# Optimization experiments

Measured on AMD Instinct MI355X. Metric: run time of the kernel, lower is better.

The kernel has to match this reference:

```python
import math
import jax, jax.numpy as jnp
import numpy as np

HIDDEN = 1024
HEADS = 16
HEAD_DIM = HIDDEN // HEADS
PRIME = 7
MAX_ITERS = 10
ENT_THRESH = 0.2
PRIME_SCALE = 1.0 / math.sqrt(PRIME * HEAD_DIM)
EPS = 1e-6


def setup_inputs() -> dict:
    key = jax.random.key(0)
    ks = jax.random.split(key, 6)
    B, S = 2, 2048
    w = 0.02
    return {
        "hidden_states": jax.random.normal(ks[0], (B, S, HIDDEN), jnp.float32),
        "q_w": jax.random.normal(ks[1], (HIDDEN, HIDDEN), jnp.float32) * w,
        "q_b": jnp.zeros((HIDDEN,), jnp.float32),
        "k_w": jax.random.normal(ks[2], (HIDDEN, HIDDEN), jnp.float32) * w,
        "k_b": jnp.zeros((HIDDEN,), jnp.float32),
        "v_w": jax.random.normal(ks[3], (HIDDEN, HIDDEN), jnp.float32) * w,
        "v_b": jnp.zeros((HIDDEN,), jnp.float32),
        "o_w": jax.random.normal(ks[4], (HIDDEN, HIDDEN), jnp.float32) * w,
        "o_b": jnp.zeros((HIDDEN,), jnp.float32),
        "attention_mask": jnp.ones((B, S), jnp.int32),
    }


def _split_heads(x):
    B, S, _ = x.shape
    return x.reshape(B, S, HEADS, HEAD_DIM).transpose(0, 2, 1, 3)


def reference(hidden_states, q_w, q_b, k_w, k_b, v_w, v_b, o_w, o_b, attention_mask):
    B, S, _ = hidden_states.shape
    # projections (torch Linear: x @ W^T + b)
    q = _split_heads(hidden_states @ q_w.T + q_b) * PRIME_SCALE  # [B,H,S,hd]
    k = _split_heads(hidden_states @ k_w.T + k_b)
    v = _split_heads(hidden_states @ v_w.T + v_b)

    scores = jnp.einsum("bhqd,bhkd->bhqk", q, k)  # [B,H,S,S]
    mask = attention_mask[:, None, None, :]
    scores = jnp.where(mask == 0, -jnp.inf, scores)
    attn = jax.nn.softmax(scores, axis=-1)  # dropout p=0 (eval)

    base = jnp.einsum("bhqk,bhkd->bhqd", attn, v)  # attention_weights @ v

    # entropy of the (fixed) attention weights: [B,H]
    entropy = -jnp.sum(attn * jnp.log(attn + EPS), axis=-1).mean(axis=-1)
    avg_entropy = entropy.mean()

    # loop never changes attn, so entropy is constant: either break at i=1 or run all
    full = base
    for i in range(1, MAX_ITERS):
        blend = 1.0 / (1.0 + math.exp(-i / MAX_ITERS))          # sigmoid(i/max)
        res_scale = 0.5 + 0.5 * blend                            # resonance scale
        full = (1.0 - blend) * full + blend * (res_scale * base)

    out_heads = jnp.where(avg_entropy < ENT_THRESH, base, full)  # [B,H,S,hd]

    merged = out_heads.transpose(0, 2, 1, 3).reshape(B, S, HIDDEN)
    return merged @ o_w.T + o_b
```

## Files before the change

kernel.cpp:

```cpp
#include <hip/hip_runtime.h>
#include <hip/hip_bf16.h>
#include <stdint.h>


#define PRIME_SCALE 0.047245559126654356f
#define LOG2E       1.4426950408889634f
#define LN2         0.6931471805599453f
#define QSCALE      (PRIME_SCALE * LOG2E)
#define BLEND_C     0.85096556f

#if __has_builtin(__builtin_amdgcn_exp2f)
#define EXP2(x) __builtin_amdgcn_exp2f(x)
#else
#define EXP2(x) exp2f(x)
#endif

typedef __attribute__((ext_vector_type(8))) short short8;
typedef __attribute__((ext_vector_type(4))) float f32x4;

__device__ __forceinline__ unsigned short f2bf(float x) {
    union { float f; unsigned int u; } v; v.f = x;
    unsigned int r = (v.u + 0x7fffu + ((v.u >> 16) & 1u)) >> 16;
    return (unsigned short)r;
}
__device__ __forceinline__ unsigned short f2bf_fast(float x) {
    union { float f; unsigned int u; } v; v.f = x;
    return (unsigned short)((v.u + 0x8000u) >> 16);
}
__device__ __forceinline__ float bf2f(unsigned short x) {
    union { unsigned int u; float f; } v; v.u = ((unsigned int)x) << 16;
    return v.f;
}
__device__ __forceinline__ unsigned cvtpk_bf16(float lo, float hi) {
    unsigned r;
    asm("v_cvt_pk_bf16_f32 %0, %1, %2" : "=v"(r) : "v"(lo), "v"(hi));
    return r;
}

__device__ __forceinline__ void glds16(const unsigned short* g, unsigned short* l) {
    __builtin_amdgcn_global_load_lds((const __attribute__((address_space(1))) unsigned int*)g,
                                     (__attribute__((address_space(3))) unsigned int*)l,
                                     16, 0, 0);
}

__global__ void zero_out_f32(float* p, int n) {
    int i = blockIdx.x * 256 + threadIdx.x;
    if (i < n) p[i] = 0.f;
}

__global__ __launch_bounds__(256) void cvt5(
    const float* __restrict__ s0, const float* __restrict__ s1, const float* __restrict__ s2,
    const float* __restrict__ s3, const float* __restrict__ s4,
    unsigned short* __restrict__ d0, unsigned short* __restrict__ d1, unsigned short* __restrict__ d2,
    unsigned short* __restrict__ d3, unsigned short* __restrict__ d4, float* entp)
{
    if (blockIdx.x == 0 && threadIdx.x == 0) entp[0] = 0.f;
    unsigned int i = blockIdx.x * 256 + threadIdx.x;
    const float* s; unsigned short* d; unsigned int off;
    if (i < (1u << 20)) { s = s0; d = d0; off = i; }
    else {
        unsigned int j = i - (1u << 20);
        unsigned int sel = j >> 18; off = j & 0x3FFFFu;
        s = sel == 0 ? s1 : sel == 1 ? s2 : sel == 2 ? s3 : s4;
        d = sel == 0 ? d1 : sel == 1 ? d2 : sel == 2 ? d3 : d4;
    }
    float4 v = ((const float4*)s)[off];
    ushort4 p; p.x = f2bf(v.x); p.y = f2bf(v.y); p.z = f2bf(v.z); p.w = f2bf(v.w);
    ((ushort4*)d)[off] = p;
}

__global__ __launch_bounds__(256) void gemm_qkv(
    const unsigned short* __restrict__ hsb,
    const unsigned short* __restrict__ qwb, const unsigned short* __restrict__ kwb,
    const unsigned short* __restrict__ vwb,
    const float* __restrict__ qb, const float* __restrict__ kb, const float* __restrict__ vb,
    unsigned short* __restrict__ Qo, unsigned short* __restrict__ Ko, unsigned short* __restrict__ Vto)
{
    const int bid = blockIdx.x;
    const int op = bid >> 8, local = bid & 255;
    const unsigned short *A, *B; const float* bias; unsigned short* C;
    int m0, n0, ldc, biasRow; float scale;
    if (op == 0)      { A = hsb; B = qwb; bias = qb; C = Qo;  m0 = (local >> 3) * 128; n0 = (local & 7) * 128;  ldc = 1024; biasRow = 0; scale = QSCALE; }
    else if (op == 1) { A = hsb; B = kwb; bias = kb; C = Ko;  m0 = (local >> 3) * 128; n0 = (local & 7) * 128;  ldc = 1024; biasRow = 0; scale = 1.f; }
    else              { A = vwb; B = hsb; bias = vb; C = Vto; m0 = (local >> 5) * 128; n0 = (local & 31) * 128; ldc = 4096; biasRow = 1; scale = 1.f; }

    __shared__ unsigned short As[128 * 32];
    __shared__ unsigned short Bs[128 * 32];
    const int t = threadIdx.x, lane = t & 63, w = t >> 6;
    const int quad = lane >> 4, l15 = lane & 15;
    const int wr = (w >> 1) * 64, wc = (w & 1) * 64;
    const int srow = lane >> 2, scol = (lane & 3) * 8;

    f32x4 acc[4][4];
#pragma unroll
    for (int i = 0; i < 4; ++i)
#pragma unroll
        for (int j = 0; j < 4; ++j) acc[i][j] = (f32x4){0.f, 0.f, 0.f, 0.f};

    for (int kk = 0; kk < 32; ++kk) {
        const int k0 = kk * 32;
#pragma unroll
        for (int j = 0; j < 2; ++j) {
            int row = (w * 2 + j) * 16 + srow;
            glds16(&A[(size_t)(m0 + row) * 1024 + k0 + scol], &As[(w * 2 + j) * 512]);
            glds16(&B[(size_t)(n0 + row) * 1024 + k0 + scol], &Bs[(w * 2 + j) * 512]);
        }
        __syncthreads();
        short8 af[4], bf[4];
#pragma unroll
        for (int mt = 0; mt < 4; ++mt) af[mt] = *(const short8*)&As[(wr + mt * 16 + l15) * 32 + quad * 8];
#pragma unroll
        for (int nt = 0; nt < 4; ++nt) bf[nt] = *(const short8*)&Bs[(wc + nt * 16 + l15) * 32 + quad * 8];
#pragma unroll
        for (int mt = 0; mt < 4; ++mt)
#pragma unroll
            for (int nt = 0; nt < 4; ++nt)
                acc[mt][nt] = __builtin_amdgcn_mfma_f32_16x16x32_bf16(af[mt], bf[nt], acc[mt][nt], 0, 0, 0);
        __syncthreads();
    }
#pragma unroll
    for (int mt = 0; mt < 4; ++mt) {
#pragma unroll
        for (int nt = 0; nt < 4; ++nt) {
            int n = n0 + wc + nt * 16 + l15;
#pragma unroll
            for (int r = 0; r < 4; ++r) {
                int m = m0 + wr + mt * 16 + quad * 4 + r;
                float bval = biasRow ? bias[m] : bias[n];
                C[(size_t)m * ldc + n] = f2bf((acc[mt][nt][r] + bval) * scale);
            }
        }
    }
}

__global__ __launch_bounds__(256, 2) void flash_split(
    const unsigned short* __restrict__ Q,
    const unsigned short* __restrict__ K,
    const unsigned short* __restrict__ Vt,
    const int* __restrict__ mask,
    unsigned short* __restrict__ O0, unsigned short* __restrict__ O1,
    float* __restrict__ lpart, float* __restrict__ Tpart)
{
    const int qt = blockIdx.x;
    const int bh = blockIdx.y;
    const int z  = blockIdx.z;
    const int b = bh >> 4, h = bh & 15;
    const int t = threadIdx.x, lane = t & 63, w = t >> 6;
    const int quad = lane >> 4, l15 = lane & 15;
    const int r8 = lane >> 3, ch8 = lane & 7;
    const int kt0 = z * 16, kt1 = kt0 + 16;
    unsigned short* __restrict__ Opart = z ? O1 : O0;

    __shared__ unsigned short Qs[256 * 64];
    __shared__ unsigned short Ks[2][64 * 64];
    __shared__ unsigned short Vs[2][64 * 64];

    const int* maskb = mask + b * 2048;

    {
        const int row0 = w * 16;
#pragma unroll
        for (int i = 0; i < 2; ++i) {
            int row = row0 + i * 8 + r8;
            int c = ch8 ^ (row & 7);
            glds16(&K[(size_t)(b * 2048 + kt0 * 64 + row) * 1024 + h * 64 + c * 8], &Ks[0][(row0 + i * 8) * 64]);
            glds16(&Vt[(size_t)(h * 64 + row) * 4096 + b * 2048 + kt0 * 64 + c * 8], &Vs[0][(row0 + i * 8) * 64]);
        }
    }
#pragma unroll
    for (int i = 0; i < 8; ++i) {
        int f = i * 256 + t; int row = f >> 3, c = f & 7;
        uint4 v = *(const uint4*)&Q[(size_t)(b * 2048 + qt * 256 + row) * 1024 + h * 64 + c * 8];
        int rx = row & 15;
        uint2 plo; plo.x = v.x; plo.y = v.y;
        uint2 phi; phi.x = v.z; phi.y = v.w;
        *(uint2*)&Qs[row * 64 + (((2 * c) ^ rx) << 2)]     = plo;
        *(uint2*)&Qs[row * 64 + (((2 * c + 1) ^ rx) << 2)] = phi;
    }
    __syncthreads();

    short8 qa[4][2];
#pragma unroll
    for (int st = 0; st < 4; ++st) {
        int prow = (w * 64 + st * 16 + l15) * 64;
#pragma unroll
        for (int hf = 0; hf < 2; ++hf) {
            int p0 = hf * 8 + quad * 2;
            union { uint2 u2[2]; short8 s8; } uu;
            uu.u2[0] = *(const uint2*)&Qs[prow + ((p0 ^ l15) << 2)];
            uu.u2[1] = *(const uint2*)&Qs[prow + (((p0 + 1) ^ l15) << 2)];
            qa[st][hf] = uu.s8;
        }
    }
    unsigned short* Ps = Qs;

    float l_r[4] = {0.f, 0.f, 0.f, 0.f}, T_r[4] = {0.f, 0.f, 0.f, 0.f};
    f32x4 o_acc[4][4];
#pragma unroll
    for (int st = 0; st < 4; ++st)
#pragma unroll
        for (int nt = 0; nt < 4; ++nt) o_acc[st][nt] = (f32x4){0.f, 0.f, 0.f, 0.f};

    int mv = maskb[kt0 * 64 + lane];

    for (int kt = kt0; kt < kt1; ++kt) {
        const int cur = kt & 1;
        int mv_next = 0;
        if (kt < kt1 - 1) {
            const int kn = (kt + 1) * 64;
            const int row0 = w * 16;
#pragma unroll
            for (int i = 0; i < 2; ++i) {
                int row = row0 + i * 8 + r8;
                int c = ch8 ^ (row & 7);
                glds16(&K[(size_t)(b * 2048 + kn + row) * 1024 + h * 64 + c * 8], &Ks[cur ^ 1][(row0 + i * 8) * 64]);
                glds16(&Vt[(size_t)(h * 64 + row) * 4096 + b * 2048 + kn + c * 8], &Vs[cur ^ 1][(row0 + i * 8) * 64]);
            }
            mv_next = maskb[kn + 64 + lane - 64];
        }
        unsigned long long bal = __ballot(mv != 0);
        unsigned mwA = (unsigned)bal, mwB = (unsigned)(bal >> 32);

#pragma unroll
        for (int nt = 0; nt < 4; ++nt) {
            int krow = nt * 16 + l15;
            short8 kf0 = *(const short8*)&Ks[cur][krow * 64 + ((quad ^ (krow & 7)) * 8)];
            short8 kf1 = *(const short8*)&Ks[cur][krow * 64 + (((quad + 4) ^ (krow & 7)) * 8)];
            f32x4 sv[4];
            __builtin_amdgcn_s_setprio(1);
#pragma unroll
            for (int st = 0; st < 4; ++st) {
                sv[st] = __builtin_amdgcn_mfma_f32_16x16x32_bf16(kf0, qa[st][0], (f32x4){0.f, 0.f, 0.f, 0.f}, 0, 0, 0);
                sv[st] = __builtin_amdgcn_mfma_f32_16x16x32_bf16(kf1, qa[st][1], sv[st], 0, 0, 0);
            }
            __builtin_amdgcn_s_setprio(0);
            unsigned mw = (nt & 2) ? mwB : mwA;
            unsigned mb = (mw >> (((nt & 1) << 4) + (quad << 2))) & 0xFu;
#pragma unroll
            for (int st = 0; st < 4; ++st) {
                float s0 = (mb & 1u) ? sv[st][0] : -1.0e30f;
                float s1 = (mb & 2u) ? sv[st][1] : -1.0e30f;
                float s2 = (mb & 4u) ? sv[st][2] : -1.0e30f;
                float s3 = (mb & 8u) ? sv[st][3] : -1.0e30f;
                float p0 = EXP2(s0), p1 = EXP2(s1), p2 = EXP2(s2), p3 = EXP2(s3);
                l_r[st] += (p0 + p1) + (p2 + p3);
                T_r[st] += (p0 * s0 + p1 * s1) + (p2 * s2 + p3 * s3);
                uint2 pk;
                pk.x = cvtpk_bf16(p0, p1);
                pk.y = cvtpk_bf16(p2, p3);
                *(uint2*)&Ps[(w * 64 + st * 16 + l15) * 64 + (((nt * 4 + quad) ^ l15) << 2)] = pk;
            }
        }

#pragma unroll
        for (int ks = 0; ks < 2; ++ks) {
            short8 pa[4];
#pragma unroll
            for (int st = 0; st < 4; ++st) {
                int prow = (w * 64 + st * 16 + l15) * 64;
                int p0 = ks * 8 + quad * 2;
                union { uint2 u2[2]; short8 s8; } uu;
                uu.u2[0] = *(const uint2*)&Ps[prow + ((p0 ^ l15) << 2)];
                uu.u2[1] = *(const uint2*)&Ps[prow + (((p0 + 1) ^ l15) << 2)];
                pa[st] = uu.s8;
            }
            __builtin_amdgcn_s_setprio(1);
#pragma unroll
            for (int nt = 0; nt < 4; ++nt) {
                int vrow = nt * 16 + l15;
                short8 vf = *(const short8*)&Vs[cur][vrow * 64 + ((((ks * 4 + quad)) ^ (vrow & 7)) * 8)];
#pragma unroll
                for (int st = 0; st < 4; ++st)
                    o_acc[st][nt] = __builtin_amdgcn_mfma_f32_16x16x32_bf16(pa[st], vf, o_acc[st][nt], 0, 0, 0);
            }
            __builtin_amdgcn_s_setprio(0);
        }
        __syncthreads();
        mv = mv_next;
    }

#pragma unroll
    for (int st = 0; st < 4; ++st) {
        float l = l_r[st], T = T_r[st];
        l += __shfl_xor(l, 16); T += __shfl_xor(T, 16);
        l += __shfl_xor(l, 32); T += __shfl_xor(T, 32);
        if (lane < 16) {
            int qrow = qt * 256 + w * 64 + st * 16 + l15;
            int li = z * 65536 + bh * 2048 + qrow;
            lpart[li] = l; Tpart[li] = T;
        }
#pragma unroll
        for (int r = 0; r < 4; ++r) {
            int mrow = b * 2048 + qt * 256 + w * 64 + st * 16 + quad * 4 + r;
#pragma unroll
            for (int nt = 0; nt < 4; ++nt)
                Opart[(size_t)mrow * 1024 + h * 64 + nt * 16 + l15] = f2bf_fast(o_acc[st][nt][r]);
        }
    }
}

__global__ __launch_bounds__(256) void combine_split(
    unsigned short* __restrict__ O0, const unsigned short* __restrict__ O1,
    const float* __restrict__ lpart)
{
    unsigned idx = blockIdx.x * 256 + threadIdx.x;
    int mrow = idx >> 8;
    int c4 = (idx & 255) << 2;
    int h = c4 >> 6;
    int b = mrow >> 11, qrow = mrow & 2047;
    int li = (b * 16 + h) * 2048 + qrow;
    float l = lpart[li] + lpart[65536 + li];
    float inv = 1.0f / l;

    ushort4 a = ((const ushort4*)O0)[idx];
    ushort4 c = ((const ushort4*)O1)[idx];
    ushort4 o;
    o.x = f2bf_fast((bf2f(a.x) + bf2f(c.x)) * inv);
    o.y = f2bf_fast((bf2f(a.y) + bf2f(c.y)) * inv);
    o.z = f2bf_fast((bf2f(a.z) + bf2f(c.z)) * inv);
    o.w = f2bf_fast((bf2f(a.w) + bf2f(c.w)) * inv);
    ((ushort4*)O0)[idx] = o;
}

__global__ __launch_bounds__(256) void entropy_k(
    const float* __restrict__ lpart, const float* __restrict__ Tpart,
    float* __restrict__ entp)
{
    __shared__ float wsum[4];
    int idx = blockIdx.x * 256 + threadIdx.x;
    float acc = 0.f;
#pragma unroll
    for (int i = 0; i < 4; ++i) {
        int r = idx * 4 + i;
        float l = lpart[r] + lpart[65536 + r];
        float T = Tpart[r] + Tpart[65536 + r];
        acc += __log2f(l) - T / l;
    }
    acc += __shfl_xor(acc, 1);
    acc += __shfl_xor(acc, 2);
    acc += __shfl_xor(acc, 4);
    acc += __shfl_xor(acc, 8);
    acc += __shfl_xor(acc, 16);
    acc += __shfl_xor(acc, 32);
    int lane = threadIdx.x & 63, w = threadIdx.x >> 6;
    if (lane == 0) wsum[w] = acc;
    __syncthreads();
    if (threadIdx.x == 0)
        atomicAdd(entp, LN2 * (wsum[0] + wsum[1] + wsum[2] + wsum[3]));
}

__global__ __launch_bounds__(256) void gemm_out_bf(
    const unsigned short* __restrict__ A, const unsigned short* __restrict__ Bw,
    const float* __restrict__ bias, const float* __restrict__ entp,
    float* __restrict__ C)
{
    const float avg = entp[0] * (1.0f / 65536.0f);
    const float scale = (avg < 0.2f) ? 1.0f : BLEND_C;

    const int m0 = blockIdx.x * 128;
    const int n0 = blockIdx.y * 64;
    __shared__ unsigned short As[128 * 32];
    __shared__ unsigned short Bs[64 * 32];
    const int t = threadIdx.x, lane = t & 63, w = t >> 6;
    const int quad = lane >> 4, l15 = lane & 15;
    const int wr = (w >> 1) * 64, wc = (w & 1) * 32;
    const int srow = lane >> 2, scol = (lane & 3) * 8;

    f32x4 acc[4][2];
#pragma unroll
    for (int i = 0; i < 4; ++i)
#pragma unroll
        for (int j = 0; j < 2; ++j) acc[i][j] = (f32x4){0.f, 0.f, 0.f, 0.f};

    for (int kk = 0; kk < 32; ++kk) {
        const int k0 = kk * 32;
#pragma unroll
        for (int j = 0; j < 2; ++j) {
            int row = (w * 2 + j) * 16 + srow;
            glds16(&A[(size_t)(m0 + row) * 1024 + k0 + scol], &As[(w * 2 + j) * 512]);
        }
        {
            int row = w * 16 + srow;
            glds16(&Bw[(size_t)(n0 + row) * 1024 + k0 + scol], &Bs[w * 512]);
        }
        __syncthreads();
        short8 af[4], bf[2];
#pragma unroll
        for (int mt = 0; mt < 4; ++mt) af[mt] = *(const short8*)&As[(wr + mt * 16 + l15) * 32 + quad * 8];
#pragma unroll
        for (int nt = 0; nt < 2; ++nt) bf[nt] = *(const short8*)&Bs[(wc + nt * 16 + l15) * 32 + quad * 8];
#pragma unroll
        for (int mt = 0; mt < 4; ++mt)
#pragma unroll
            for (int nt = 0; nt < 2; ++nt)
                acc[mt][nt] = __builtin_amdgcn_mfma_f32_16x16x32_bf16(af[mt], bf[nt], acc[mt][nt], 0, 0, 0);
        __syncthreads();
    }
#pragma unroll
    for (int mt = 0; mt < 4; ++mt) {
#pragma unroll
        for (int nt = 0; nt < 2; ++nt) {
            int n = n0 + wc + nt * 16 + l15;
#pragma unroll
            for (int r = 0; r < 4; ++r) {
                int m = m0 + wr + mt * 16 + quad * 4 + r;
                C[(size_t)m * 1024 + n] = scale * acc[mt][nt][r] + bias[n];
            }
        }
    }
}

extern "C" void kernel_launch(void* const* d_in, const int* in_sizes, int n_in,
                              void* d_out, int out_size, void* d_ws, size_t ws_size,
                              hipStream_t stream)
{
    const float* hs = (const float*)d_in[0];
    const float* qw = (const float*)d_in[1];
    const float* qb = (const float*)d_in[2];
    const float* kw = (const float*)d_in[3];
    const float* kb = (const float*)d_in[4];
    const float* vw = (const float*)d_in[5];
    const float* vb = (const float*)d_in[6];
    const float* ow = (const float*)d_in[7];
    const float* ob = (const float*)d_in[8];
    const int*   mask = (const int*)d_in[9];
    float* out = (float*)d_out;

    const size_t MB = 1024 * 1024;
    char* ws = (char*)d_ws;
    dim3 blk(256);

    if (ws_size >= 50 * MB) {
        unsigned short* hsb = (unsigned short*)(ws);
        unsigned short* Q   = (unsigned short*)(ws + 8 * MB);
        unsigned short* Kp  = (unsigned short*)(ws + 16 * MB);
        unsigned short* Vt  = (unsigned short*)(ws + 24 * MB);
        unsigned short* qwb = (unsigned short*)(ws + 32 * MB);
        unsigned short* kwb = (unsigned short*)(ws + 34 * MB);
        unsigned short* vwb = (unsigned short*)(ws + 36 * MB);
        unsigned short* owb = (unsigned short*)(ws + 38 * MB);
        float* entp         = (float*)(ws + 40 * MB);
        unsigned short* Op1 = (unsigned short*)(ws + 41 * MB);
        float* lpart        = (float*)(ws + 49 * MB);
        float* Tpart        = (float*)(ws + 49 * MB + 524288);
        unsigned short* Op0 = hsb;

        cvt5<<<dim3(8192), blk, 0, stream>>>(hs, qw, kw, vw, ow, hsb, qwb, kwb, vwb, owb, entp);
        gemm_qkv<<<dim3(768), blk, 0, stream>>>(hsb, qwb, kwb, vwb, qb, kb, vb, Q, Kp, Vt);
        flash_split<<<dim3(8, 32, 2), blk, 0, stream>>>(Q, Kp, Vt, mask, Op0, Op1, lpart, Tpart);
        combine_split<<<dim3(4096), blk, 0, stream>>>(Op0, Op1, lpart);
        entropy_k<<<dim3(64), blk, 0, stream>>>(lpart, Tpart, entp);
        gemm_out_bf<<<dim3(32, 16), blk, 0, stream>>>(Op0, owb, ob, entp, out);
    } else {
        zero_out_f32<<<dim3((out_size + 255) / 256), blk, 0, stream>>>(out, out_size);
    }
}
```

Baseline: 204.4 us.

## Keep P in registers via permlane swaps and specialize unmasked softmax path

The softmax probabilities are no longer written to LDS and read back for the PV MFMA. Instead they stay in registers and are rearranged into the A-operand layout with v_permlane32_swap and v_permlane16_swap instructions. A separate fully-unmasked path is added that skips the per-element mask selects when the whole 64-key tile is valid. This removes the LDS round trip for P and its bank traffic, at the cost of extra registers and code size from the duplicated macro body.

```diff
diff --git a/kernel.cpp b/kernel.cpp
--- a/kernel.cpp
+++ b/kernel.cpp
@@ -133,6 +133,43 @@
     }
 }
 
+
+#define QK_SOFTMAX(MASKED)                                                          \
+    _Pragma("unroll")                                                               \
+    for (int nt = 0; nt < 4; ++nt) {                                                \
+        int krow = nt * 16 + l15;                                                   \
+        short8 kf0 = *(const short8*)&Ks[cur][krow * 64 + ((quad ^ (krow & 7)) * 8)];       \
+        short8 kf1 = *(const short8*)&Ks[cur][krow * 64 + (((quad + 4) ^ (krow & 7)) * 8)]; \
+        f32x4 sv[4];                                                                \
+        __builtin_amdgcn_s_setprio(1);                                              \
+        _Pragma("unroll")                                                           \
+        for (int st = 0; st < 4; ++st) {                                            \
+            sv[st] = __builtin_amdgcn_mfma_f32_16x16x32_bf16(kf0, qa[st][0], (f32x4){0.f, 0.f, 0.f, 0.f}, 0, 0, 0); \
+            sv[st] = __builtin_amdgcn_mfma_f32_16x16x32_bf16(kf1, qa[st][1], sv[st], 0, 0, 0); \
+        }                                                                           \
+        __builtin_amdgcn_s_setprio(0);                                              \
+        unsigned mb = 0xFu;                                                         \
+        if (MASKED) {                                                               \
+            unsigned mw = (nt & 2) ? mwB : mwA;                                     \
+            mb = (mw >> (((nt & 1) << 4) + (quad << 2))) & 0xFu;                    \
+        }                                                                           \
+        _Pragma("unroll")                                                           \
+        for (int st = 0; st < 4; ++st) {                                            \
+            float s0 = sv[st][0], s1 = sv[st][1], s2 = sv[st][2], s3 = sv[st][3];   \
+            if (MASKED) {                                                           \
+                s0 = (mb & 1u) ? s0 : -1.0e30f;                                     \
+                s1 = (mb & 2u) ? s1 : -1.0e30f;                                     \
+                s2 = (mb & 4u) ? s2 : -1.0e30f;                                     \
+                s3 = (mb & 8u) ? s3 : -1.0e30f;                                     \
+            }                                                                       \
+            float p0 = EXP2(s0), p1 = EXP2(s1), p2 = EXP2(s2), p3 = EXP2(s3);       \
+            l_r[st] += (p0 + p1) + (p2 + p3);                                       \
+            T_r[st] += (p0 * s0 + p1 * s1) + (p2 * s2 + p3 * s3);                   \
+            pk[nt][st][0] = cvtpk_bf16(p0, p1);                                     \
+            pk[nt][st][1] = cvtpk_bf16(p2, p3);                                     \
+        }                                                                           \
+    }
+
 __global__ __launch_bounds__(256, 2) void flash_split(
     const unsigned short* __restrict__ Q,
     const unsigned short* __restrict__ K,
@@ -192,7 +229,6 @@
             qa[st][hf] = uu.s8;
         }
     }
-    unsigned short* Ps = Qs;
 
     float l_r[4] = {0.f, 0.f, 0.f, 0.f}, T_r[4] = {0.f, 0.f, 0.f, 0.f};
     f32x4 o_acc[4][4];
@@ -216,40 +252,16 @@
                 glds16(&K[(size_t)(b * 2048 + kn + row) * 1024 + h * 64 + c * 8], &Ks[cur ^ 1][(row0 + i * 8) * 64]);
                 glds16(&Vt[(size_t)(h * 64 + row) * 4096 + b * 2048 + kn + c * 8], &Vs[cur ^ 1][(row0 + i * 8) * 64]);
             }
-            mv_next = maskb[kn + 64 + lane - 64];
+            mv_next = maskb[kn + lane];
         }
         unsigned long long bal = __ballot(mv != 0);
         unsigned mwA = (unsigned)bal, mwB = (unsigned)(bal >> 32);
 
-#pragma unroll
-        for (int nt = 0; nt < 4; ++nt) {
-            int krow = nt * 16 + l15;
-            short8 kf0 = *(const short8*)&Ks[cur][krow * 64 + ((quad ^ (krow & 7)) * 8)];
-            short8 kf1 = *(const short8*)&Ks[cur][krow * 64 + (((quad + 4) ^ (krow & 7)) * 8)];
-            f32x4 sv[4];
-            __builtin_amdgcn_s_setprio(1);
-#pragma unroll
-            for (int st = 0; st < 4; ++st) {
-                sv[st] = __builtin_amdgcn_mfma_f32_16x16x32_bf16(kf0, qa[st][0], (f32x4){0.f, 0.f, 0.f, 0.f}, 0, 0, 0);
-                sv[st] = __builtin_amdgcn_mfma_f32_16x16x32_bf16(kf1, qa[st][1], sv[st], 0, 0, 0);
-            }
-            __builtin_amdgcn_s_setprio(0);
-            unsigned mw = (nt & 2) ? mwB : mwA;
-            unsigned mb = (mw >> (((nt & 1) << 4) + (quad << 2))) & 0xFu;
-#pragma unroll
-            for (int st = 0; st < 4; ++st) {
-                float s0 = (mb & 1u) ? sv[st][0] : -1.0e30f;
-                float s1 = (mb & 2u) ? sv[st][1] : -1.0e30f;
-                float s2 = (mb & 4u) ? sv[st][2] : -1.0e30f;
-                float s3 = (mb & 8u) ? sv[st][3] : -1.0e30f;
-                float p0 = EXP2(s0), p1 = EXP2(s1), p2 = EXP2(s2), p3 = EXP2(s3);
-                l_r[st] += (p0 + p1) + (p2 + p3);
-                T_r[st] += (p0 * s0 + p1 * s1) + (p2 * s2 + p3 * s3);
-                uint2 pk;
-                pk.x = cvtpk_bf16(p0, p1);
-                pk.y = cvtpk_bf16(p2, p3);
-                *(uint2*)&Ps[(w * 64 + st * 16 + l15) * 64 + (((nt * 4 + quad) ^ l15) << 2)] = pk;
-            }
+        unsigned pk[4][4][2];
+        if ((mwA & mwB) == 0xFFFFFFFFu) {
+            QK_SOFTMAX(0)
+        } else {
+            QK_SOFTMAX(1)
         }
 
 #pragma unroll
@@ -257,11 +269,14 @@
             short8 pa[4];
 #pragma unroll
             for (int st = 0; st < 4; ++st) {
-                int prow = (w * 64 + st * 16 + l15) * 64;
-                int p0 = ks * 8 + quad * 2;
-                union { uint2 u2[2]; short8 s8; } uu;
-                uu.u2[0] = *(const uint2*)&Ps[prow + ((p0 ^ l15) << 2)];
-                uu.u2[1] = *(const uint2*)&Ps[prow + (((p0 + 1) ^ l15) << 2)];
+                unsigned a0 = pk[2 * ks][st][0], a1 = pk[2 * ks][st][1];
+                unsigned b0 = pk[2 * ks + 1][st][0], b1 = pk[2 * ks + 1][st][1];
+                asm("v_permlane32_swap_b32 %0, %1" : "+v"(a0), "+v"(b0));
+                asm("v_permlane32_swap_b32 %0, %1" : "+v"(a1), "+v"(b1));
+                asm("v_permlane16_swap_b32 %0, %1" : "+v"(a0), "+v"(b0));
+                asm("v_permlane16_swap_b32 %0, %1" : "+v"(a1), "+v"(b1));
+                union { unsigned u[4]; short8 s8; } uu;
+                uu.u[0] = a0; uu.u[1] = a1; uu.u[2] = b0; uu.u[3] = b1;
                 pa[st] = uu.s8;
             }
             __builtin_amdgcn_s_setprio(1);
```

After: 205.1 us. No clear change (+0.4%).
